# Kernel optimization log

Measured on AMD Instinct MI355X. Metric: run time of the kernel, lower is better.

Reference implementation:

```python
import jax, jax.numpy as jnp
import numpy as np


def setup_inputs() -> dict:
    key = jax.random.key(0)
    k1, k2, k3 = jax.random.split(key, 3)
    N, P, C = 4, 1024, 3
    H, W = 128, 128
    # coordinates in pixel space: x in [0, W), y in [0, H)
    coords01 = jax.random.uniform(k1, (N, P, 2), dtype=jnp.float32)
    coordinates = coords01 * jnp.array([W, H], dtype=jnp.float32)
    values = jax.random.normal(k2, (N, P, C), dtype=jnp.float32)
    # sigma in [1.0, 3.0), one std per batch element
    sigma = 1.0 + 2.0 * jax.random.uniform(k3, (N, 1), dtype=jnp.float32)
    return {
        "coordinates": coordinates,
        "values": values,
        "sigma": sigma,
        "height": H,
        "width": W,
    }


def reference(coordinates, values, sigma, height, width):
    # coordinates: [N, P, 2] (x, y); values: [N, P, C]; sigma: [N, 1]
    dt = coordinates.dtype
    ys = jnp.arange(height, dtype=dt)  # [H]
    xs = jnp.arange(width, dtype=dt)   # [W]
    x = coordinates[..., 0]            # [N, P]
    y = coordinates[..., 1]            # [N, P]
    # squared distance from each point to each grid cell: [N, P, H, W]
    dy2 = (ys[None, None, :, None] - y[:, :, None, None]) ** 2  # [N,P,H,1]
    dx2 = (xs[None, None, None, :] - x[:, :, None, None]) ** 2  # [N,P,1,W]
    dist2 = dy2 + dx2                                           # [N,P,H,W]
    inv_two_sigma2 = 0.5 / (sigma ** 2)                         # [N,1]
    weight = jnp.exp(-dist2 * inv_two_sigma2[:, :, None, None])  # [N,P,H,W]
    # scatter-add each point's gaussian-weighted value onto the grid
    out = jnp.einsum('nphw,npc->nchw', weight, values)  # [N,C,H,W]
    return out
```

## Files before the change

### kernel.cpp

```cpp
#include <hip/hip_runtime.h>
#include <hip/hip_bf16.h>


#define MAINBLOCK 1024
#define NSEG 8

__device__ __forceinline__ float fast_exp2(float x) {
#if __has_builtin(__builtin_amdgcn_exp2f)
    return __builtin_amdgcn_exp2f(x);
#else
    return exp2f(x);
#endif
}

__global__ __launch_bounds__(256) void splat2d_prep(
    const float* __restrict__ coords,
    const float* __restrict__ vals,
    const float* __restrict__ sigma,
    float*       __restrict__ packed,
    int P, int total)
{
    const int idx = blockIdx.x * 256 + threadIdx.x;
    if (idx >= total) return;
    const int n = idx / P;
    const float sg = sigma[n];
    const float s  = -1.44269504088896f * 0.5f / (sg * sg);
    const float x  = coords[(size_t)idx * 2 + 0];
    const float y  = coords[(size_t)idx * 2 + 1];
    const float v0 = vals[(size_t)idx * 3 + 0];
    const float v1 = vals[(size_t)idx * 3 + 1];
    const float v2 = vals[(size_t)idx * 3 + 2];
    float4* o = (float4*)(packed + (size_t)idx * 8);
    o[0] = make_float4(-2.0f * s * x, -2.0f * s * y, s * fmaf(x, x, y * y), v0);
    o[1] = make_float4(v1, v2, 0.0f, 0.0f);
}

__global__ __launch_bounds__(MAINBLOCK) void splat2d_row_sgpr(
    const float* __restrict__ packed,
    const float* __restrict__ sigma,
    float*       __restrict__ out,
    int P, int H)
{
    __shared__ float red0[MAINBLOCK];
    __shared__ float red1[MAINBLOCK];
    __shared__ float red2[MAINBLOCK];

    const int n   = blockIdx.x / H;
    const int h   = blockIdx.x % H;
    const int tid = threadIdx.x;
    const int px  = tid & 127;
    const int seg = __builtin_amdgcn_readfirstlane(tid >> 7);

    const float sg = sigma[n];
    const float s  = -1.44269504088896f * 0.5f / (sg * sg);
    const float fh = (float)h;
    const float fx = (float)px;
    const float bb = s * fmaf(fx, fx, fh * fh);

    const int PS = P / NSEG;
    const float* __restrict__ sp =
        packed + ((size_t)n * P + (size_t)(seg * PS)) * 8;

    float a0 = 0.f, a1 = 0.f, a2 = 0.f;

#pragma unroll 4
    for (int i = 0; i < PS; ++i) {
        const float4 qa = *(const float4*)(sp + 8 * i);
        const float4 qb = *(const float4*)(sp + 8 * i + 4);
        const float  t  = fmaf(qa.y, fh, bb);
        const float  e  = fmaf(qa.x, fx, t + qa.z);
        const float  wg = fast_exp2(e);
        a0 = fmaf(wg, qa.w, a0);
        a1 = fmaf(wg, qb.x, a1);
        a2 = fmaf(wg, qb.y, a2);
    }

    red0[tid] = a0; red1[tid] = a1; red2[tid] = a2;
    __syncthreads();

    if (tid < 128) {
        float s0 = 0.f, s1 = 0.f, s2 = 0.f;
#pragma unroll
        for (int k = 0; k < NSEG; ++k) {
            s0 += red0[tid + 128 * k];
            s1 += red1[tid + 128 * k];
            s2 += red2[tid + 128 * k];
        }
        const size_t hw   = (size_t)H * 128;
        const size_t base = ((size_t)n * 3) * hw + (size_t)h * 128 + tid;
        out[base]          = s0;
        out[base + hw]     = s1;
        out[base + 2 * hw] = s2;
    }
}

__global__ __launch_bounds__(MAINBLOCK) void splat2d_row_raw(
    const float* __restrict__ coords, const float* __restrict__ vals,
    const float* __restrict__ sigma, float* __restrict__ out, int P, int H)
{
    __shared__ float red0[MAINBLOCK];
    __shared__ float red1[MAINBLOCK];
    __shared__ float red2[MAINBLOCK];

    const int n   = blockIdx.x / H;
    const int h   = blockIdx.x % H;
    const int tid = threadIdx.x;
    const int px  = tid & 127;
    const int seg = __builtin_amdgcn_readfirstlane(tid >> 7);

    const float sg = sigma[n];
    const float s  = -1.44269504088896f * 0.5f / (sg * sg);
    const float fh = (float)h;
    const float fx = (float)px;

    const int PS = P / NSEG;
    const int p0 = seg * PS;
    const float* __restrict__ cp = coords + ((size_t)n * P + p0) * 2;
    const float* __restrict__ vp = vals   + ((size_t)n * P + p0) * 3;

    float a0 = 0.f, a1 = 0.f, a2 = 0.f;

#pragma unroll 4
    for (int i = 0; i < PS; ++i) {
        const float x  = cp[2 * i + 0];
        const float y  = cp[2 * i + 1];
        const float v0 = vp[3 * i + 0];
        const float v1 = vp[3 * i + 1];
        const float v2 = vp[3 * i + 2];
        const float dx = x - fx;
        const float dy = y - fh;
        const float e  = s * fmaf(dx, dx, dy * dy);
        const float wg = fast_exp2(e);
        a0 = fmaf(wg, v0, a0);
        a1 = fmaf(wg, v1, a1);
        a2 = fmaf(wg, v2, a2);
    }

    red0[tid] = a0; red1[tid] = a1; red2[tid] = a2;
    __syncthreads();

    if (tid < 128) {
        float s0 = 0.f, s1 = 0.f, s2 = 0.f;
#pragma unroll
        for (int k = 0; k < NSEG; ++k) {
            s0 += red0[tid + 128 * k];
            s1 += red1[tid + 128 * k];
            s2 += red2[tid + 128 * k];
        }
        const size_t hw   = (size_t)H * 128;
        const size_t base = ((size_t)n * 3) * hw + (size_t)h * 128 + tid;
        out[base]          = s0;
        out[base + hw]     = s1;
        out[base + 2 * hw] = s2;
    }
}

#define BLOCK 256
#define SEGS  8

__global__ __launch_bounds__(BLOCK) void splat2d_lds(
    const float* __restrict__ coords, const float* __restrict__ vals,
    const float* __restrict__ sigma, const int* __restrict__ wptr,
    float* __restrict__ out, int P, int pixPerN, int blocksPerN, int nSeg)
{
    const int PS_MAX = 1024;
    __shared__ float4 ptA[PS_MAX / SEGS];
    __shared__ float2 ptB[PS_MAX / SEGS];

    const int W = *wptr;
    int t = blockIdx.x;
    const int seg = t % nSeg;  t /= nSeg;
    const int n   = t / blocksPerN;
    const int blk = t % blocksPerN;

    const float sg = sigma[n];
    const float s  = -1.44269504088896f * 0.5f / (sg * sg);

    const int PS = P / nSeg;
    const int p0 = seg * PS;
    const float* __restrict__ cp = coords + ((size_t)n * P + p0) * 2;
    const float* __restrict__ vp = vals   + ((size_t)n * P + p0) * 3;

    for (int p = threadIdx.x; p < PS; p += BLOCK) {
        const float x  = cp[2 * p + 0];
        const float y  = cp[2 * p + 1];
        const float c  = s * fmaf(x, x, y * y);
        ptA[p] = make_float4(x, y, c, vp[3 * p + 0]);
        ptB[p] = make_float2(vp[3 * p + 1], vp[3 * p + 2]);
    }
    __syncthreads();

    const int pix = blk * BLOCK + threadIdx.x;
    const int h = pix / W;
    const int w = pix - h * W;
    const float fx = (float)w, fy = (float)h;
    const float tx = -2.0f * s * fx, ty = -2.0f * s * fy;
    const float bb = s * fmaf(fx, fx, fy * fy);

    float a0 = 0.f, a1 = 0.f, a2 = 0.f;
#pragma unroll 8
    for (int p = 0; p < PS; ++p) {
        const float4 q = ptA[p];
        const float2 r = ptB[p];
        const float e = fmaf(tx, q.x, fmaf(ty, q.y, bb + q.z));
        const float wgt = fast_exp2(e);
        a0 = fmaf(wgt, q.w, a0);
        a1 = fmaf(wgt, r.x, a1);
        a2 = fmaf(wgt, r.y, a2);
    }

    const size_t base = ((size_t)n * 3) * (size_t)pixPerN + (size_t)pix;
    unsafeAtomicAdd(&out[base],                       a0);
    unsafeAtomicAdd(&out[base + (size_t)pixPerN],     a1);
    unsafeAtomicAdd(&out[base + 2 * (size_t)pixPerN], a2);
}

extern "C" void kernel_launch(void* const* d_in, const int* in_sizes, int n_in,
                              void* d_out, int out_size, void* d_ws, size_t ws_size,
                              hipStream_t stream) {
    const float* coords = (const float*)d_in[0];
    const float* vals   = (const float*)d_in[1];
    const float* sigma  = (const float*)d_in[2];
    const int* hptr = (const int*)d_in[3];
    const int* wptr = (const int*)d_in[4];

    const int N = in_sizes[2];
    const int P = in_sizes[0] / (2 * N);
    const int C = in_sizes[1] / (N * P);
    const int pixPerN = out_size / (N * C);

    float* out = (float*)d_out;

    if (pixPerN == 16384 && P <= 1024 && (P % NSEG) == 0 && C == 3) {
        const int H = 128;
        const int total = N * P;
        const size_t need = (size_t)total * 8 * sizeof(float);
        if (d_ws != nullptr && ws_size >= need) {
            splat2d_prep<<<(total + 255) / 256, 256, 0, stream>>>(
                coords, vals, sigma, (float*)d_ws, P, total);
            splat2d_row_sgpr<<<N * H, MAINBLOCK, 0, stream>>>(
                (const float*)d_ws, sigma, out, P, H);
        } else {
            splat2d_row_raw<<<N * H, MAINBLOCK, 0, stream>>>(
                coords, vals, sigma, out, P, H);
        }
        (void)hptr; (void)wptr;
    } else {
        const int nSeg = (P % SEGS == 0 && P <= 1024) ? SEGS : 1;
        const int blocksPerN = pixPerN / BLOCK;
        const int grid = N * blocksPerN * nSeg;
        hipMemsetAsync(out, 0, (size_t)out_size * sizeof(float), stream);
        splat2d_lds<<<grid, BLOCK, 0, stream>>>(coords, vals, sigma, wptr,
                                                out, P, pixPerN, blocksPerN, nSeg);
    }
}
```

Baseline: 82.01 us.

## Drop prep kernel; fold sigma scaling into raw-input row splat kernel

Removes the packing prep kernel and its workspace round-trip, so the row-splat kernel reads coordinates and values directly in a single launch. The exponent is rewritten as -(r·dx)^2-(r·dy)^2 with r = sqrt(log2(e)/2)/sigma, so each point needs two FMAs for the scaled offsets plus one for the sum. The loop unroll goes from 4 to 8. This saves a launch and a global write/read pass, at the cost of unaligned scalar loads of the 2- and 3-float records instead of float4 loads.

```diff
diff --git a/kernel.cpp b/kernel.cpp
--- a/kernel.cpp
+++ b/kernel.cpp
@@ -13,30 +13,9 @@
 #endif
 }
 
-__global__ __launch_bounds__(256) void splat2d_prep(
+__global__ __launch_bounds__(MAINBLOCK) void splat2d_row_raw(
     const float* __restrict__ coords,
     const float* __restrict__ vals,
-    const float* __restrict__ sigma,
-    float*       __restrict__ packed,
-    int P, int total)
-{
-    const int idx = blockIdx.x * 256 + threadIdx.x;
-    if (idx >= total) return;
-    const int n = idx / P;
-    const float sg = sigma[n];
-    const float s  = -1.44269504088896f * 0.5f / (sg * sg);
-    const float x  = coords[(size_t)idx * 2 + 0];
-    const float y  = coords[(size_t)idx * 2 + 1];
-    const float v0 = vals[(size_t)idx * 3 + 0];
-    const float v1 = vals[(size_t)idx * 3 + 1];
-    const float v2 = vals[(size_t)idx * 3 + 2];
-    float4* o = (float4*)(packed + (size_t)idx * 8);
-    o[0] = make_float4(-2.0f * s * x, -2.0f * s * y, s * fmaf(x, x, y * y), v0);
-    o[1] = make_float4(v1, v2, 0.0f, 0.0f);
-}
-
-__global__ __launch_bounds__(MAINBLOCK) void splat2d_row_sgpr(
-    const float* __restrict__ packed,
     const float* __restrict__ sigma,
     float*       __restrict__ out,
     int P, int H)
@@ -52,66 +31,11 @@
     const int seg = __builtin_amdgcn_readfirstlane(tid >> 7);
 
     const float sg = sigma[n];
-    const float s  = -1.44269504088896f * 0.5f / (sg * sg);
+    const float r  = 0.84932180028802f / sg;
     const float fh = (float)h;
     const float fx = (float)px;
-    const float bb = s * fmaf(fx, fx, fh * fh);
-
-    const int PS = P / NSEG;
-    const float* __restrict__ sp =
-        packed + ((size_t)n * P + (size_t)(seg * PS)) * 8;
-
-    float a0 = 0.f, a1 = 0.f, a2 = 0.f;
-
-#pragma unroll 4
-    for (int i = 0; i < PS; ++i) {
-        const float4 qa = *(const float4*)(sp + 8 * i);
-        const float4 qb = *(const float4*)(sp + 8 * i + 4);
-        const float  t  = fmaf(qa.y, fh, bb);
-        const float  e  = fmaf(qa.x, fx, t + qa.z);
-        const float  wg = fast_exp2(e);
-        a0 = fmaf(wg, qa.w, a0);
-        a1 = fmaf(wg, qb.x, a1);
-        a2 = fmaf(wg, qb.y, a2);
-    }
-
-    red0[tid] = a0; red1[tid] = a1; red2[tid] = a2;
-    __syncthreads();
-
-    if (tid < 128) {
-        float s0 = 0.f, s1 = 0.f, s2 = 0.f;
-#pragma unroll
-        for (int k = 0; k < NSEG; ++k) {
-            s0 += red0[tid + 128 * k];
-            s1 += red1[tid + 128 * k];
-            s2 += red2[tid + 128 * k];
-        }
-        const size_t hw   = (size_t)H * 128;
-        const size_t base = ((size_t)n * 3) * hw + (size_t)h * 128 + tid;
-        out[base]          = s0;
-        out[base + hw]     = s1;
-        out[base + 2 * hw] = s2;
-    }
-}
-
-__global__ __launch_bounds__(MAINBLOCK) void splat2d_row_raw(
-    const float* __restrict__ coords, const float* __restrict__ vals,
-    const float* __restrict__ sigma, float* __restrict__ out, int P, int H)
-{
-    __shared__ float red0[MAINBLOCK];
-    __shared__ float red1[MAINBLOCK];
-    __shared__ float red2[MAINBLOCK];
-
-    const int n   = blockIdx.x / H;
-    const int h   = blockIdx.x % H;
-    const int tid = threadIdx.x;
-    const int px  = tid & 127;
-    const int seg = __builtin_amdgcn_readfirstlane(tid >> 7);
-
-    const float sg = sigma[n];
-    const float s  = -1.44269504088896f * 0.5f / (sg * sg);
-    const float fh = (float)h;
-    const float fx = (float)px;
+    const float nrfx = -r * fx;
+    const float nrfh = -r * fh;
 
     const int PS = P / NSEG;
     const int p0 = seg * PS;
@@ -120,16 +44,16 @@
 
     float a0 = 0.f, a1 = 0.f, a2 = 0.f;
 
-#pragma unroll 4
+#pragma unroll 8
     for (int i = 0; i < PS; ++i) {
         const float x  = cp[2 * i + 0];
         const float y  = cp[2 * i + 1];
         const float v0 = vp[3 * i + 0];
         const float v1 = vp[3 * i + 1];
         const float v2 = vp[3 * i + 2];
-        const float dx = x - fx;
-        const float dy = y - fh;
-        const float e  = s * fmaf(dx, dx, dy * dy);
+        const float u  = fmaf(r, x, nrfx);
+        const float w  = fmaf(r, y, nrfh);
+        const float e  = fmaf(u, -u, -w * w);
         const float wg = fast_exp2(e);
         a0 = fmaf(wg, v0, a0);
         a1 = fmaf(wg, v1, a1);
@@ -233,18 +157,9 @@
 
     if (pixPerN == 16384 && P <= 1024 && (P % NSEG) == 0 && C == 3) {
         const int H = 128;
-        const int total = N * P;
-        const size_t need = (size_t)total * 8 * sizeof(float);
-        if (d_ws != nullptr && ws_size >= need) {
-            splat2d_prep<<<(total + 255) / 256, 256, 0, stream>>>(
-                coords, vals, sigma, (float*)d_ws, P, total);
-            splat2d_row_sgpr<<<N * H, MAINBLOCK, 0, stream>>>(
-                (const float*)d_ws, sigma, out, P, H);
-        } else {
-            splat2d_row_raw<<<N * H, MAINBLOCK, 0, stream>>>(
-                coords, vals, sigma, out, P, H);
-        }
-        (void)hptr; (void)wptr;
+        splat2d_row_raw<<<N * H, MAINBLOCK, 0, stream>>>(
+            coords, vals, sigma, out, P, H);
+        (void)hptr; (void)wptr; (void)d_ws; (void)ws_size;
     } else {
         const int nSeg = (P % SEGS == 0 && P <= 1024) ? SEGS : 1;
         const int blocksPerN = pixPerN / BLOCK;
```

Result: faster. 78.38 us (-4.4%).
